# Kernel tuning notes

Hardware: AMD Instinct MI355X
Metric: run time of the kernel (lower is better)

## Reference

```python
import jax, jax.numpy as jnp
import numpy as np

N, D = 320, 256
TEMP = 2.0

# case ids sorted: [-11,-10,-1,0,1,10,11]; value order: [0,1,2,3,11,12,13]
CASE_VALS = jnp.array([-11, -10, -1, 0, 1, 10, 11], dtype=jnp.int32)
TABLE = jnp.array([
    [0, 2, 2, 1, 1, 0, 1],   # case -11
    [0, 2, 2, 2, 2, 2, 2],   # case -10
    [0, 2, 2, 2, 1, 0, 2],   # case -1
    [0, 2, 2, 2, 2, 2, 2],   # case 0
    [0, 2, 2, 2, 1, 2, 2],   # case 1
    [0, 2, 2, 2, 2, 0, 2],   # case 10
    [0, 2, 2, 1, 1, 0, 1],   # case 11
], dtype=jnp.int32)


def setup_inputs() -> dict:
    key = jax.random.key(0)
    k1, k2, k3 = jax.random.split(key, 3)
    features = jax.random.normal(k1, (N, D), dtype=jnp.float32)
    y_times = jax.random.uniform(k2, (N,), dtype=jnp.float32)
    y_events = jax.random.randint(k3, (N,), 0, 2, dtype=jnp.int32)
    return {"features": features, "y_times": y_times, "y_events": y_events}


def _forward(features, y_times, y_events):
    n = features.shape[0]
    # pairwise -L2 similarity / temperature  (safe sqrt: diag is 0)
    diff = features[:, None, :] - features[None, :, :]          # [N,N,D]
    d2 = jnp.sum(diff * diff, axis=-1)                           # [N,N]
    norm = jnp.where(d2 > 0, jnp.sqrt(jnp.where(d2 > 0, d2, 1.0)), 0.0)
    logits = -norm / TEMP
    logits = logits - jax.lax.stop_gradient(jnp.max(logits, axis=1, keepdims=True))
    exp_logits = jnp.exp(logits)

    idx = jnp.arange(n)
    eye = idx[:, None] == idx[None, :]

    def per_anchor(k):
        pld = y_times - y_times[k]                               # [N]
        abs_i = jnp.abs(pld)[:, None]                            # |pld[i]|
        pj = pld[None, :]                                        # pld[j]
        # sequential torch mask assignments collapse to this piecewise map
        td = jnp.where(pj > abs_i, 3,
             jnp.where(-pj > abs_i, 1,
             jnp.where(jnp.abs(pj) > 0, 2, 0))).astype(jnp.int32)
        td = jnp.where(eye, 0, td)                               # fill_diagonal_(0)
        neg = jnp.where(td != 0, y_events[None, :] * 10 + td, 0) # {0,1,2,3,11,12,13}
        sgn = jnp.sign(pld).astype(jnp.int32)
        cid = (y_events + 10 * y_events[k]) * sgn                # per-row case id
        cidx = jnp.searchsorted(CASE_VALS, cid)                  # [N]
        vidx = jnp.where(neg > 3, neg - 7, neg)                  # map vals to 0..6
        mapped = TABLE[cidx[:, None], vidx]                      # numba lookup, fused
        final = (mapped == 1).astype(jnp.float32) + 0.5 * (mapped == 2)
        keep = (idx != k).astype(jnp.float32)                    # delete row/col k
        final = final * keep[:, None] * keep[None, :]
        valid = jnp.sum(final, axis=-1) > 0                      # [N]
        Np = jnp.sum(valid)
        denom = jnp.sum(final * exp_logits, axis=-1)             # masked sum-exp
        logp = logits[:, k] - jnp.log(jnp.where(valid, denom, 1.0))
        loss_k = -jnp.sum(jnp.where(valid, logp, 0.0)) / jnp.maximum(Np, 1)
        return jnp.where(Np > 0, loss_k, 0.0), (Np > 0)

    losses, has_pos = jax.vmap(per_anchor)(idx)
    return jnp.sum(losses) / jnp.sum(has_pos)


def reference(features, y_times, y_events):
    return _forward(features, y_times, y_events)
```

## Files before the change

### kernel.cpp

```cpp
#include <hip/hip_runtime.h>
#include <math.h>

#define NN 320
#define DD 256
#define PS 328

__device__ __constant__ unsigned int c_PACK[7] =
    {0x2294u, 0x1554u, 0x1254u, 0x1554u, 0x1654u, 0x1154u, 0x2294u};

__global__ __launch_bounds__(256) void prep_kernel(
    const float* __restrict__ F, const float* __restrict__ yt,
    const int* __restrict__ ye, float4* __restrict__ FT4,
    float4* __restrict__ meta) {
    __shared__ float sh[64 * 65];
    const int b = blockIdx.x;
    if (b < 20) {
        float (*tile)[65] = (float(*)[65])sh;
        const int I = b % 5;
        const int J = b / 5;
        const int lane = threadIdx.x & 63;
        const int quad = threadIdx.x >> 6;
#pragma unroll
        for (int r0 = 0; r0 < 64; r0 += 4) {
            const int r = r0 + quad;
            tile[r][lane] = F[(I * 64 + r) * DD + J * 64 + lane];
        }
        __syncthreads();
#pragma unroll
        for (int q = 0; q < 16; q += 4) {
            const int d4 = q + quad;
            float4 v = make_float4(tile[lane][d4 * 4 + 0], tile[lane][d4 * 4 + 1],
                                   tile[lane][d4 * 4 + 2], tile[lane][d4 * 4 + 3]);
            FT4[(J * 16 + d4) * NN + I * 64 + lane] = v;
        }
    } else {
        float* s_t = sh;
        for (int j = threadIdx.x; j < NN; j += 256) s_t[j] = yt[j];
        __syncthreads();
        for (int j = threadIdx.x; j < NN; j += 256) {
            const float tj = s_t[j];
            int lt = 0, le = 0, pos = 0;
            for (int l = 0; l < NN; ++l) {
                const float tl = s_t[l];
                lt  += (tl < tj);
                le  += (tl <= tj);
                pos += (tl < tj) || (tl == tj && l < j);
            }
            meta[j] = make_float4(tj, __int_as_float(lt), __int_as_float(le),
                                  __int_as_float(pos | (ye[j] << 16)));
        }
    }
}

__global__ __launch_bounds__(NN) void pair_scan_kernel(
    const float* __restrict__ F, const float4* __restrict__ FT4,
    const float4* __restrict__ meta, float* __restrict__ L,
    float* __restrict__ P0, float* __restrict__ P1) {
    __shared__ __align__(16) float fi[DD];
    __shared__ float A0[2][NN];
    __shared__ float A1[2][NN];
    const int i = blockIdx.x;
    const int j = threadIdx.x;
    if (j < DD) fi[j] = F[i * DD + j];
    __syncthreads();

    const float4* __restrict__ fi4 = (const float4*)fi;
    float a0 = 0.f, a1 = 0.f, a2 = 0.f, a3 = 0.f;
#pragma unroll 8
    for (int d4 = 0; d4 < DD / 4; ++d4) {
        const float4 f4 = fi4[d4];
        const float4 g4 = FT4[d4 * NN + j];
        const float u0 = f4.x - g4.x, u1 = f4.y - g4.y;
        const float u2 = f4.z - g4.z, u3 = f4.w - g4.w;
        a0 = fmaf(u0, u0, a0);
        a1 = fmaf(u1, u1, a1);
        a2 = fmaf(u2, u2, a2);
        a3 = fmaf(u3, u3, a3);
    }
    const float d2 = (a0 + a1) + (a2 + a3);
    const float nrm = (d2 > 0.f) ? sqrtf(d2) : 0.f;
    const float lg = -0.5f * nrm;
    L[i * NN + j] = lg;
    const float e = expf(lg);

    const int pe  = __float_as_int(meta[j].w);
    const int pos = pe & 0xFFFF;
    const int ev  = pe >> 16;
    A0[0][pos] = ev ? 0.f : e;
    A1[0][pos] = ev ? e : 0.f;
    __syncthreads();

    int src = 0;
#pragma unroll
    for (int off = 1; off < NN; off <<= 1) {
        const int dst = src ^ 1;
        float v0 = A0[src][j], v1 = A1[src][j];
        if (j >= off) { v0 += A0[src][j - off]; v1 += A1[src][j - off]; }
        A0[dst][j] = v0;
        A1[dst][j] = v1;
        __syncthreads();
        src = dst;
    }

    P0[i * PS + j] = (j == 0) ? 0.f : A0[src][j - 1];
    P1[i * PS + j] = (j == 0) ? 0.f : A1[src][j - 1];
    if (j == NN - 1) {
        P0[i * PS + NN] = A0[src][j];
        P1[i * PS + NN] = A1[src][j];
    }
}

__global__ __launch_bounds__(NN) void anchor_kernel(
    const float4* __restrict__ meta, const float* __restrict__ L,
    const float* __restrict__ P0, const float* __restrict__ P1,
    float* __restrict__ accv) {
    __shared__ float swl[5];
    __shared__ float swn[5];
    const int k = blockIdx.x;
    const int i = threadIdx.x;
    const int wave = i >> 6, lane = i & 63;

    const float4 mk = meta[k];
    const float4 mi = meta[i];
    const float tk = mk.x, ti = mi.x;
    const int rlt_k = __float_as_int(mk.y), rle_k = __float_as_int(mk.z);
    const int evk   = __float_as_int(mk.w) >> 16;
    const int rlt_i = __float_as_int(mi.y), rle_i = __float_as_int(mi.z);
    const int evi   = __float_as_int(mi.w) >> 16;

    const int sgn = (ti > tk) ? 1 : ((ti < tk) ? -1 : 0);
    const unsigned pack = c_PACK[3 + sgn * (evi + 2 * evk)];
    const int rlo = min(rlt_i, rlt_k);
    const int rhi = max(rle_i, rle_k);

    const float* __restrict__ b0 = P0 + i * PS;
    const float* __restrict__ b1 = P1 + i * PS;
    const float q0lo = b0[rlo], q0hi = b0[rhi], q0a = b0[rlt_k], q0b = b0[rle_k], t0 = b0[NN];
    const float q1lo = b1[rlo], q1hi = b1[rhi], q1a = b1[rlt_k], q1b = b1[rle_k], t1 = b1[NN];

    const float LO0 = q0lo, HI0 = t0 - q0hi, MI0 = q0hi - q0lo - (q0b - q0a);
    const float LO1 = q1lo, HI1 = t1 - q1hi, MI1 = q1hi - q1lo - (q1b - q1a);

    const float c1 = (float)((pack >> 2) & 3u),  c2 = (float)((pack >> 4) & 3u);
    const float c3 = (float)((pack >> 6) & 3u),  c4 = (float)((pack >> 8) & 3u);
    const float c5 = (float)((pack >> 10) & 3u), c6 = (float)((pack >> 12) & 3u);

    float dx = c1 * LO0 + c2 * MI0 + c3 * HI0 + c4 * LO1 + c5 * MI1 + c6 * HI1;
    if (ti != tk) dx -= (float)((pack >> (2 * (2 + 3 * evi))) & 3u);

    float lp = 0.f, np = 0.f;
    if (i != k && dx > 0.f) {
        lp = L[k * NN + i] - logf(0.5f * dx);
        np = 1.f;
    }
#pragma unroll
    for (int off = 32; off > 0; off >>= 1) {
        lp += __shfl_down(lp, off);
        np += __shfl_down(np, off);
    }
    if (lane == 0) { swl[wave] = lp; swn[wave] = np; }
    __syncthreads();
    if (i == 0) {
        float s = 0.f, n = 0.f;
#pragma unroll
        for (int w = 0; w < 5; ++w) { s += swl[w]; n += swn[w]; }
        accv[k] = s;
        accv[NN + k] = n;
    }
}

__global__ __launch_bounds__(NN) void finalize_kernel(
    const float* __restrict__ accv, float* __restrict__ out) {
    __shared__ float s_l[5];
    __shared__ float s_h[5];
    const int k = threadIdx.x;
    const int wave = k >> 6, lane = k & 63;
    const float np = accv[NN + k];
    float loss = (np > 0.f) ? (-accv[k] / np) : 0.f;
    float has  = (np > 0.f) ? 1.f : 0.f;
#pragma unroll
    for (int off = 32; off > 0; off >>= 1) {
        loss += __shfl_down(loss, off);
        has  += __shfl_down(has, off);
    }
    if (lane == 0) { s_l[wave] = loss; s_h[wave] = has; }
    __syncthreads();
    if (k == 0) {
        float tl = 0.f, th = 0.f;
#pragma unroll
        for (int w = 0; w < 5; ++w) { tl += s_l[w]; th += s_h[w]; }
        out[0] = tl / th;
    }
}

extern "C" void kernel_launch(void* const* d_in, const int* in_sizes, int n_in,
                              void* d_out, int out_size, void* d_ws, size_t ws_size,
                              hipStream_t stream) {
    const float* F  = (const float*)d_in[0];
    const float* yt = (const float*)d_in[1];
    const int*   ye = (const int*)d_in[2];
    float* out = (float*)d_out;
    float* ws  = (float*)d_ws;

    float4* meta = (float4*)ws;
    float4* FT4  = (float4*)(ws + 4 * NN);
    float*  L    = ws + 4 * NN + 4 * (DD / 4) * NN;
    float*  P0   = L + NN * NN;
    float*  P1   = P0 + NN * PS;
    float*  accv = P1 + NN * PS;

    prep_kernel<<<21, 256, 0, stream>>>(F, yt, ye, FT4, meta);
    pair_scan_kernel<<<NN, NN, 0, stream>>>(F, FT4, meta, L, P0, P1);
    anchor_kernel<<<NN, NN, 0, stream>>>(meta, L, P0, P1, accv);
    finalize_kernel<<<1, NN, 0, stream>>>(accv, out);
}
```

Before: 94.32 us.

## Fuse pair, scan, anchor and finalize kernels using atomics and last-block ticket

```diff
diff --git a/kernel.cpp b/kernel.cpp
--- a/kernel.cpp
+++ b/kernel.cpp
@@ -3,7 +3,6 @@
 
 #define NN 320
 #define DD 256
-#define PS 328
 
 __device__ __constant__ unsigned int c_PACK[7] =
     {0x2294u, 0x1554u, 0x1254u, 0x1554u, 0x1654u, 0x1154u, 0x2294u};
@@ -11,15 +10,17 @@
 __global__ __launch_bounds__(256) void prep_kernel(
     const float* __restrict__ F, const float* __restrict__ yt,
     const int* __restrict__ ye, float4* __restrict__ FT4,
-    float4* __restrict__ meta) {
+    float4* __restrict__ meta, float* __restrict__ acc) {
     __shared__ float sh[64 * 65];
+    __shared__ int rr[3][4][64];
     const int b = blockIdx.x;
+    const int tid = threadIdx.x;
     if (b < 20) {
         float (*tile)[65] = (float(*)[65])sh;
         const int I = b % 5;
         const int J = b / 5;
-        const int lane = threadIdx.x & 63;
-        const int quad = threadIdx.x >> 6;
+        const int lane = tid & 63;
+        const int quad = tid >> 6;
 #pragma unroll
         for (int r0 = 0; r0 < 64; r0 += 4) {
             const int r = r0 + quad;
@@ -33,35 +34,59 @@
                                    tile[lane][d4 * 4 + 2], tile[lane][d4 * 4 + 3]);
             FT4[(J * 16 + d4) * NN + I * 64 + lane] = v;
         }
-    } else {
+    } else if (b < 25) {
         float* s_t = sh;
-        for (int j = threadIdx.x; j < NN; j += 256) s_t[j] = yt[j];
+        for (int l = tid; l < NN; l += 256) s_t[l] = yt[l];
         __syncthreads();
-        for (int j = threadIdx.x; j < NN; j += 256) {
-            const float tj = s_t[j];
-            int lt = 0, le = 0, pos = 0;
-            for (int l = 0; l < NN; ++l) {
-                const float tl = s_t[l];
-                lt  += (tl < tj);
-                le  += (tl <= tj);
-                pos += (tl < tj) || (tl == tj && l < j);
+        const int jj = tid & 63;
+        const int q  = tid >> 6;
+        const int j  = (b - 20) * 64 + jj;
+        const float tj = s_t[j];
+        int lt = 0, le = 0, pos = 0;
+        const int l0 = q * 80;
+        for (int l = l0; l < l0 + 80; ++l) {
+            const float tl = s_t[l];
+            lt  += (tl < tj);
+            le  += (tl <= tj);
+            pos += (tl < tj) || (tl == tj && l < j);
+        }
+        rr[0][q][jj] = lt; rr[1][q][jj] = le; rr[2][q][jj] = pos;
+        __syncthreads();
+        if (q == 0) {
+#pragma unroll
+            for (int w = 1; w < 4; ++w) {
+                lt += rr[0][w][jj]; le += rr[1][w][jj]; pos += rr[2][w][jj];
             }
             meta[j] = make_float4(tj, __int_as_float(lt), __int_as_float(le),
                                   __int_as_float(pos | (ye[j] << 16)));
         }
+    } else {
+        for (int t = tid; t < 2 * NN + 1; t += 256) acc[t] = 0.f;
     }
 }
 
-__global__ __launch_bounds__(NN) void pair_scan_kernel(
+__global__ __launch_bounds__(NN) void fused_kernel(
     const float* __restrict__ F, const float4* __restrict__ FT4,
-    const float4* __restrict__ meta, float* __restrict__ L,
-    float* __restrict__ P0, float* __restrict__ P1) {
+    const float4* __restrict__ meta, float* __restrict__ acc,
+    float* __restrict__ out) {
     __shared__ __align__(16) float fi[DD];
-    __shared__ float A0[2][NN];
-    __shared__ float A1[2][NN];
+    __shared__ float S0[NN + 1];
+    __shared__ float S1[NN + 1];
+    __shared__ float w0[5], w1[5];
+    __shared__ float4 smi;
+    __shared__ int s_done;
+
+    float* __restrict__ accL = acc;
+    float* __restrict__ accN = acc + NN;
+    unsigned* ticket = (unsigned*)(acc + 2 * NN);
+
     const int i = blockIdx.x;
     const int j = threadIdx.x;
+    const int wave = j >> 6, lane = j & 63;
+
     if (j < DD) fi[j] = F[i * DD + j];
+    if (j == 0) smi = meta[i];
+    const float4 mj = meta[j];
     __syncthreads();
 
     const float4* __restrict__ fi4 = (const float4*)fi;
@@ -80,63 +105,49 @@
     const float d2 = (a0 + a1) + (a2 + a3);
     const float nrm = (d2 > 0.f) ? sqrtf(d2) : 0.f;
     const float lg = -0.5f * nrm;
-    L[i * NN + j] = lg;
     const float e = expf(lg);
 
-    const int pe  = __float_as_int(meta[j].w);
-    const int pos = pe & 0xFFFF;
-    const int ev  = pe >> 16;
-    A0[0][pos] = ev ? 0.f : e;
-    A1[0][pos] = ev ? e : 0.f;
-    __syncthreads();
-
-    int src = 0;
-#pragma unroll
-    for (int off = 1; off < NN; off <<= 1) {
-        const int dst = src ^ 1;
-        float v0 = A0[src][j], v1 = A1[src][j];
-        if (j >= off) { v0 += A0[src][j - off]; v1 += A1[src][j - off]; }
-        A0[dst][j] = v0;
-        A1[dst][j] = v1;
-        __syncthreads();
-        src = dst;
-    }
-
-    P0[i * PS + j] = (j == 0) ? 0.f : A0[src][j - 1];
-    P1[i * PS + j] = (j == 0) ? 0.f : A1[src][j - 1];
-    if (j == NN - 1) {
-        P0[i * PS + NN] = A0[src][j];
-        P1[i * PS + NN] = A1[src][j];
-    }
-}
-
-__global__ __launch_bounds__(NN) void anchor_kernel(
-    const float4* __restrict__ meta, const float* __restrict__ L,
-    const float* __restrict__ P0, const float* __restrict__ P1,
-    float* __restrict__ accv) {
-    __shared__ float swl[5];
-    __shared__ float swn[5];
-    const int k = blockIdx.x;
-    const int i = threadIdx.x;
-    const int wave = i >> 6, lane = i & 63;
-
-    const float4 mk = meta[k];
-    const float4 mi = meta[i];
-    const float tk = mk.x, ti = mi.x;
-    const int rlt_k = __float_as_int(mk.y), rle_k = __float_as_int(mk.z);
-    const int evk   = __float_as_int(mk.w) >> 16;
+    const int pej = __float_as_int(mj.w);
+    const int pos = pej & 0xFFFF;
+    const int evj = pej >> 16;
+    S0[pos] = evj ? 0.f : e;
+    S1[pos] = evj ? e : 0.f;
+    __syncthreads();
+
+    float v0 = S0[j], v1 = S1[j];
+#pragma unroll
+    for (int off = 1; off < 64; off <<= 1) {
+        const float n0 = __shfl_up(v0, off);
+        const float n1 = __shfl_up(v1, off);
+        if (lane >= off) { v0 += n0; v1 += n1; }
+    }
+    if (lane == 63) { w0[wave] = v0; w1[wave] = v1; }
+    __syncthreads();
+    float p0 = 0.f, p1 = 0.f;
+#pragma unroll
+    for (int w = 0; w < 4; ++w) {
+        if (wave > w) { p0 += w0[w]; p1 += w1[w]; }
+    }
+    v0 += p0; v1 += p1;
+    S0[j + 1] = v0; S1[j + 1] = v1;
+    if (j == 0) { S0[0] = 0.f; S1[0] = 0.f; }
+    __syncthreads();
+
+    const float4 mi = smi;
+    const float ti = mi.x;
     const int rlt_i = __float_as_int(mi.y), rle_i = __float_as_int(mi.z);
     const int evi   = __float_as_int(mi.w) >> 16;
-
-    const int sgn = (ti > tk) ? 1 : ((ti < tk) ? -1 : 0);
-    const unsigned pack = c_PACK[3 + sgn * (evi + 2 * evk)];
-    const int rlo = min(rlt_i, rlt_k);
-    const int rhi = max(rle_i, rle_k);
-
-    const float* __restrict__ b0 = P0 + i * PS;
-    const float* __restrict__ b1 = P1 + i * PS;
-    const float q0lo = b0[rlo], q0hi = b0[rhi], q0a = b0[rlt_k], q0b = b0[rle_k], t0 = b0[NN];
-    const float q1lo = b1[rlo], q1hi = b1[rhi], q1a = b1[rlt_k], q1b = b1[rle_k], t1 = b1[NN];
+    const float ta = mj.x;
+    const int rlt_a = __float_as_int(mj.y), rle_a = __float_as_int(mj.z);
+    const int eva   = evj;
+
+    const int sgn = (ti > ta) ? 1 : ((ti < ta) ? -1 : 0);
+    const unsigned pack = c_PACK[3 + sgn * (evi + 2 * eva)];
+    const int rlo = min(rlt_i, rlt_a);
+    const int rhi = max(rle_i, rle_a);
+
+    const float q0lo = S0[rlo], q0hi = S0[rhi], q0a = S0[rlt_a], q0b = S0[rle_a], t0 = S0[NN];
+    const float q1lo = S1[rlo], q1hi = S1[rhi], q1a = S1[rlt_a], q1b = S1[rle_a], t1 = S1[NN];
 
     const float LO0 = q0lo, HI0 = t0 - q0hi, MI0 = q0hi - q0lo - (q0b - q0a);
     const float LO1 = q1lo, HI1 = t1 - q1hi, MI1 = q1hi - q1lo - (q1b - q1a);
@@ -146,49 +157,37 @@
     const float c5 = (float)((pack >> 10) & 3u), c6 = (float)((pack >> 12) & 3u);
 
     float dx = c1 * LO0 + c2 * MI0 + c3 * HI0 + c4 * LO1 + c5 * MI1 + c6 * HI1;
-    if (ti != tk) dx -= (float)((pack >> (2 * (2 + 3 * evi))) & 3u);
-
-    float lp = 0.f, np = 0.f;
-    if (i != k && dx > 0.f) {
-        lp = L[k * NN + i] - logf(0.5f * dx);
-        np = 1.f;
-    }
+    if (ti != ta) dx -= (float)((pack >> (2 * (2 + 3 * evi))) & 3u);
+
+    if (i != j && dx > 0.f) {
+        atomicAdd(&accL[j], lg - logf(0.5f * dx));
+        atomicAdd(&accN[j], 1.f);
+    }
+
+    __threadfence();
+    __syncthreads();
+    if (j == 0) {
+        const unsigned old = atomicAdd(ticket, 1u);
+        s_done = (old == NN - 1);
+    }
+    __syncthreads();
+    if (!s_done) return;
+    __threadfence();
+
+    const float nj = accN[j];
+    float lossj = (nj > 0.f) ? (-accL[j] / nj) : 0.f;
+    float hasj  = (nj > 0.f) ? 1.f : 0.f;
 #pragma unroll
     for (int off = 32; off > 0; off >>= 1) {
-        lp += __shfl_down(lp, off);
-        np += __shfl_down(np, off);
-    }
-    if (lane == 0) { swl[wave] = lp; swn[wave] = np; }
-    __syncthreads();
-    if (i == 0) {
-        float s = 0.f, n = 0.f;
-#pragma unroll
-        for (int w = 0; w < 5; ++w) { s += swl[w]; n += swn[w]; }
-        accv[k] = s;
-        accv[NN + k] = n;
-    }
-}
-
-__global__ __launch_bounds__(NN) void finalize_kernel(
-    const float* __restrict__ accv, float* __restrict__ out) {
-    __shared__ float s_l[5];
-    __shared__ float s_h[5];
-    const int k = threadIdx.x;
-    const int wave = k >> 6, lane = k & 63;
-    const float np = accv[NN + k];
-    float loss = (np > 0.f) ? (-accv[k] / np) : 0.f;
-    float has  = (np > 0.f) ? 1.f : 0.f;
-#pragma unroll
-    for (int off = 32; off > 0; off >>= 1) {
-        loss += __shfl_down(loss, off);
-        has  += __shfl_down(has, off);
-    }
-    if (lane == 0) { s_l[wave] = loss; s_h[wave] = has; }
-    __syncthreads();
-    if (k == 0) {
+        lossj += __shfl_down(lossj, off);
+        hasj  += __shfl_down(hasj, off);
+    }
+    if (lane == 0) { w0[wave] = lossj; w1[wave] = hasj; }
+    __syncthreads();
+    if (j == 0) {
         float tl = 0.f, th = 0.f;
 #pragma unroll
-        for (int w = 0; w < 5; ++w) { tl += s_l[w]; th += s_h[w]; }
+        for (int w = 0; w < 5; ++w) { tl += w0[w]; th += w1[w]; }
         out[0] = tl / th;
     }
 }
@@ -204,13 +203,8 @@
 
     float4* meta = (float4*)ws;
     float4* FT4  = (float4*)(ws + 4 * NN);
-    float*  L    = ws + 4 * NN + 4 * (DD / 4) * NN;
-    float*  P0   = L + NN * NN;
-    float*  P1   = P0 + NN * PS;
-    float*  accv = P1 + NN * PS;
-
-    prep_kernel<<<21, 256, 0, stream>>>(F, yt, ye, FT4, meta);
-    pair_scan_kernel<<<NN, NN, 0, stream>>>(F, FT4, meta, L, P0, P1);
-    anchor_kernel<<<NN, NN, 0, stream>>>(meta, L, P0, P1, accv);
-    finalize_kernel<<<1, NN, 0, stream>>>(accv, out);
+    float*  acc  = ws + 4 * NN + 4 * (DD / 4) * NN;
+
+    prep_kernel<<<26, 256, 0, stream>>>(F, yt, ye, FT4, meta, acc);
+    fused_kernel<<<NN, NN, 0, stream>>>(F, FT4, meta, acc, out);
 }
```

After: 93.71 us. About the same (-0.6%).
